# Kernel tuning notes

Hardware: AMD Instinct MI355X
Metric: run time of the kernel (lower is better)

Reference implementation:

```python
import jax, jax.numpy as jnp
import numpy as np

B, IN_CAPS, IN_DIM = 64, 2048, 16
NUM_CAPS, OUT_DIM = 32, 16
NUM_ROUTING = 3


def squash(v, axis=-1):
    # scale = |v|^2 / (1 + |v|^2) / |v|  (faithful to source, no epsilon)
    s2 = jnp.sum(jnp.square(v), axis=axis, keepdims=True)
    scale = s2 / (1.0 + s2) / jnp.sqrt(s2)
    return scale * v


def setup_inputs() -> dict:
    key = jax.random.key(0)
    k1, k2 = jax.random.split(key)
    inputs = jax.random.normal(k1, (B, IN_CAPS, IN_DIM), dtype=jnp.float32)
    # glorot-ish scaled transform matrices
    W = jax.random.normal(k2, (IN_CAPS, NUM_CAPS, IN_DIM, OUT_DIM), dtype=jnp.float32) * 0.05
    return {"inputs": inputs, "W": W}


def reference(inputs, W):
    # Prediction vectors u_hat[b,i,k,:] = inputs[b,i,:] @ W[i,k,:,:]
    u_hat = jnp.einsum('bid,ikdo->biko', inputs, W)  # [B, I, K, O]
    # Routing logits b (per-batch; source initializes from zeros and accumulates agreement)
    b = jnp.zeros(u_hat.shape[:3], dtype=u_hat.dtype)  # [B, I, K]
    v = None
    for i in range(NUM_ROUTING):
        c = jax.nn.softmax(b, axis=2)                      # coupling coeffs over output caps K
        s = jnp.einsum('bik,biko->bko', c, u_hat)          # weighted sum over input caps I
        v = squash(s)                                      # [B, K, O]
        if i != NUM_ROUTING - 1:
            b = b + jnp.einsum('biko,bko->bik', u_hat, v)  # agreement update
    return v  # [B, NUM_CAPS, OUT_DIM]
```

## Files before the change

kernel.cpp:

```cpp
#include <hip/hip_runtime.h>
#include <math.h>
#include <stdint.h>

#define NB 64
#define NI 2048
#define NK 32
#define ND 16

typedef _Float16 h2t   __attribute__((ext_vector_type(2)));
typedef _Float16 f16x4 __attribute__((ext_vector_type(4)));
typedef float    f32x4 __attribute__((ext_vector_type(4)));

#if defined(__has_builtin)
#if __has_builtin(__builtin_amdgcn_global_load_lds)
#define HAVE_GLL 1
#endif
#endif
#ifndef HAVE_GLL
#define HAVE_GLL 0
#endif

static __device__ __forceinline__ uint32_t pack_h2(float a, float b) {
    h2t p; p.x = (_Float16)a; p.y = (_Float16)b;
    return __builtin_bit_cast(uint32_t, p);
}

static __device__ __forceinline__ float swz_xor16(float x) {
    int v = __builtin_amdgcn_ds_swizzle(__builtin_bit_cast(int, x), 0x401F);
    return __builtin_bit_cast(float, v);
}
static __device__ __forceinline__ float xreduce_o(float p) {
    p += swz_xor16(p);
    p += __shfl_xor(p, 32);
    return p;
}

__global__ __launch_bounds__(256)
void conv_wx(const float* __restrict__ Wg, uint32_t* __restrict__ Wh,
             const float* __restrict__ X,  uint32_t* __restrict__ XT)
{
    __shared__ float tile[32 * 264];
    const int t = threadIdx.x;
    if (blockIdx.x < 2048) {
        const int i = blockIdx.x;
        const float4* src = (const float4*)(Wg + (size_t)i * 8192);
#pragma unroll
        for (int j = 0; j < 8; ++j) {
            const int f4 = t + j * 256;
            const int k  = f4 >> 6;
            const int r4 = f4 & 63;
            *(float4*)(&tile[k * 264 + r4 * 4]) = src[f4];
        }
        __syncthreads();
        const int T  = t >> 3;
        const int l0 = (t & 7) * 8;
        const float* s = tile + T * 264;
        uint2* dst = (uint2*)(Wh + (size_t)i * 4096) + T * 64 + l0;
#pragma unroll
        for (int n = 0; n < 8; ++n) {
            const int l = l0 + n;
            const int q = l >> 4, r = l & 15;
            uint2 u;
            u.x = pack_h2(s[(4 * q + 0) * 16 + r], s[(4 * q + 1) * 16 + r]);
            u.y = pack_h2(s[(4 * q + 2) * 16 + r], s[(4 * q + 3) * 16 + r]);
            dst[n] = u;
        }
    } else {
        const int g = (blockIdx.x - 2048) * 256 + t;
        const int b = g >> 11, i = g & 2047;
        const float4* src = (const float4*)(X + ((size_t)b * 2048 + i) * 16);
        const float4 f0 = src[0], f1 = src[1], f2 = src[2], f3 = src[3];
        uint4 o0, o1;
        o0.x = pack_h2(f0.x, f0.y); o0.y = pack_h2(f0.z, f0.w);
        o0.z = pack_h2(f1.x, f1.y); o0.w = pack_h2(f1.z, f1.w);
        o1.x = pack_h2(f2.x, f2.y); o1.y = pack_h2(f2.z, f2.w);
        o1.z = pack_h2(f3.x, f3.y); o1.w = pack_h2(f3.z, f3.w);
        uint4* dst = (uint4*)(XT + (size_t)i * 512 + b * 8);
        dst[0] = o0; dst[1] = o1;
    }
}

template<int VMODE>
__global__ __launch_bounds__(256, 2)
void caps_pass_m(const uint32_t* __restrict__ XT,
                 const uint32_t* __restrict__ Wh,
                 const float* __restrict__ V,
                 uint32_t* __restrict__ part_h)
{
    constexpr int IC = 16;
    constexpr int NP = IC / 2;
    __shared__ uint32_t Ws[2][2][4096];
    __shared__ uint32_t Xs[2048];
    __shared__ float    Ep[2][4][16];

    const int t = threadIdx.x;
    const int l = t & 63;
    const int w = t >> 6;
    const int r = l & 15;
    const int q = l >> 4;

    const int wg     = blockIdx.x;
    const int xcd    = wg & 7;
    const int slot   = wg >> 3;
    const int ichunk = xcd * 16 + (slot >> 2);
    const int bg     = slot & 3;
    const int i0 = ichunk * IC;
    const int b0 = bg * 16;

    f32x4 s_acc[8];
#pragma unroll
    for (int tt = 0; tt < 8; ++tt) s_acc[tt] = (f32x4){0.f, 0.f, 0.f, 0.f};

    f32x4 v_r[8];
    if constexpr (VMODE == 1) {
#pragma unroll
        for (int tt = 0; tt < 8; ++tt)
            v_r[tt] = *(const f32x4*)(V + ((size_t)(b0 + r) * NK + (8 * w + tt)) * 16 + 4 * q);
    }

    {
        const int ig = t >> 4, uu = t & 15;
        const uint4* src = (const uint4*)(XT + (size_t)(i0 + ig) * 512 + b0 * 8);
        *(uint4*)&Xs[ig * 128 + uu * 4]        = src[uu];
        *(uint4*)&Xs[ig * 128 + (uu + 16) * 4] = src[uu + 16];
    }

#if HAVE_GLL
#define STAGE_T(sl, half, tile)                                                \
    {                                                                          \
        const size_t ibase_ = (size_t)(tile) * 4096;                           \
        _Pragma("unroll")                                                      \
        for (int jj = 0; jj < 4; ++jj) {                                       \
            const int p = w * 4 + jj;                                          \
            __builtin_amdgcn_global_load_lds(                                  \
                (const __attribute__((address_space(1))) void*)(Wh + ibase_ + p * 256 + l * 4), \
                (__attribute__((address_space(3))) void*)&Ws[sl][half][p * 256], 16, 0, 0); \
        }                                                                      \
    }
#define BAR_W(n) asm volatile("s_waitcnt vmcnt(" #n ")\ns_barrier" ::: "memory");
#else
#define STAGE_T(sl, half, tile)                                                \
    {                                                                          \
        const size_t ibase_ = (size_t)(tile) * 4096;                           \
        _Pragma("unroll")                                                      \
        for (int jj = 0; jj < 4; ++jj) {                                       \
            const int p = w * 4 + jj;                                          \
            ((uint4*)&Ws[sl][half][p * 256])[l] = *(const uint4*)(Wh + ibase_ + p * 256 + l * 4); \
        }                                                                      \
    }
#define BAR_W(n) asm volatile("s_waitcnt vmcnt(0) lgkmcnt(0)\ns_barrier" ::: "memory");
#endif
#define BAR_E() asm volatile("s_waitcnt lgkmcnt(0)\ns_barrier" ::: "memory");

    __syncthreads();

    STAGE_T(0, 0, i0 + 0) STAGE_T(0, 1, i0 + 1)
    STAGE_T(1, 0, i0 + 2) STAGE_T(1, 1, i0 + 3)

    for (int j = 0; j < NP; ++j) {
        const int s = j & 1;
        if (j == 0) { BAR_W(8) } else { BAR_W(0) }

        if (j >= 1 && j + 1 < NP) {
            const int ns = s ^ 1;
            const int nt = i0 + 2 * (j + 1);
            STAGE_T(ns, 0, nt) STAGE_T(ns, 1, nt + 1)
        }

#pragma unroll
        for (int ia = 0; ia < 2; ++ia) {
            const int ii = 2 * j + ia;
            const f16x4 xb = *(const f16x4*)&Xs[ii * 128 + r * 8 + q * 2];

            if constexpr (VMODE == 0) {
#pragma unroll
                for (int tt = 0; tt < 8; ++tt) {
                    const f16x4 a = *(const f16x4*)&Ws[s][ia][(w * 8 + tt) * 128 + l * 2];
                    s_acc[tt] = __builtin_amdgcn_mfma_f32_16x16x16f16(a, xb, s_acc[tt], 0, 0, 0);
                }
            } else {
                f32x4 um[8];
#pragma unroll
                for (int tt = 0; tt < 8; ++tt) {
                    const f16x4 a = *(const f16x4*)&Ws[s][ia][(w * 8 + tt) * 128 + l * 2];
                    um[tt] = __builtin_amdgcn_mfma_f32_16x16x16f16(
                        a, xb, (f32x4){0.f, 0.f, 0.f, 0.f}, 0, 0, 0);
                }
                float e[8];
                float esp = 0.f;
#pragma unroll
                for (int tt = 0; tt < 8; ++tt) {
                    float p = um[tt][0] * v_r[tt][0];
                    p = fmaf(um[tt][1], v_r[tt][1], p);
                    p = fmaf(um[tt][2], v_r[tt][2], p);
                    p = fmaf(um[tt][3], v_r[tt][3], p);
                    p = xreduce_o(p);
                    e[tt] = __expf(p);
                    esp += e[tt];
                }
                if (q == 0) Ep[ia][w][r] = esp;
                BAR_E();
                const float es = Ep[ia][0][r] + Ep[ia][1][r]
                               + Ep[ia][2][r] + Ep[ia][3][r];
                const float ci = __builtin_amdgcn_rcpf(es);
#pragma unroll
                for (int tt = 0; tt < 8; ++tt) {
                    const float c = e[tt] * ci;
                    s_acc[tt][0] = fmaf(c, um[tt][0], s_acc[tt][0]);
                    s_acc[tt][1] = fmaf(c, um[tt][1], s_acc[tt][1]);
                    s_acc[tt][2] = fmaf(c, um[tt][2], s_acc[tt][2]);
                    s_acc[tt][3] = fmaf(c, um[tt][3], s_acc[tt][3]);
                }
            }
        }
    }
#undef STAGE_T
#undef BAR_W
#undef BAR_E

    uint32_t* base = part_h + (size_t)(bg * 128 + ichunk) * 4096 + r * 256 + 2 * q;
#pragma unroll
    for (int tt = 0; tt < 8; ++tt) {
        uint2 st;
        st.x = pack_h2(s_acc[tt][0], s_acc[tt][1]);
        st.y = pack_h2(s_acc[tt][2], s_acc[tt][3]);
        *(uint2*)(base + (8 * w + tt) * 8) = st;
    }
}

template<int RMODE>
__global__ __launch_bounds__(256)
void caps_reduce(const uint32_t* __restrict__ part_h,
                 const float* __restrict__ S0red,
                 float* __restrict__ S0out,
                 float* __restrict__ Vout)
{
    __shared__ float2 red[4][64];
    const int t   = threadIdx.x;
    const int jl  = t & 63;
    const int qc  = t >> 6;
    const int jb  = blockIdx.x * 64;
    const int j   = jb + jl;
    const int b   = j >> 8;
    const int bg  = b >> 4;
    const int loc = (b & 15) * 256 + (j & 255);
    const uint32_t* p = part_h + ((size_t)(bg * 128 + qc * 32)) * 4096 + loc;
    float sx = 0.f, sy = 0.f;
#pragma unroll 8
    for (int ic = 0; ic < 32; ++ic) {
        h2t v = __builtin_bit_cast(h2t, p[(size_t)ic * 4096]);
        sx += (float)v.x; sy += (float)v.y;
    }
    red[qc][jl] = make_float2(sx, sy);
    __syncthreads();
    if (t < 64) {
        const int jj = jb + t;
        float2 a0 = red[0][t], a1 = red[1][t], a2 = red[2][t], a3 = red[3][t];
        const float tx = a0.x + a1.x + a2.x + a3.x;
        const float ty = a0.y + a1.y + a2.y + a3.y;
        if constexpr (RMODE == 0) {
            S0out[2 * jj]     = tx;
            S0out[2 * jj + 1] = ty;
            const float vx = tx * (1.0f / 32.0f), vy = ty * (1.0f / 32.0f);
            float sq = vx * vx + vy * vy;
#pragma unroll
            for (int mask = 4; mask >= 1; mask >>= 1) sq += __shfl_xor(sq, mask);
            const float sc = sqrtf(sq) / (1.0f + sq);
            Vout[2 * jj]     = vx * sc;
            Vout[2 * jj + 1] = vy * sc;
        } else if constexpr (RMODE == 1) {
            const float v0x = S0red[2 * jj] * (1.0f / 32.0f);
            const float v0y = S0red[2 * jj + 1] * (1.0f / 32.0f);
            float sq0 = v0x * v0x + v0y * v0y;
#pragma unroll
            for (int mask = 4; mask >= 1; mask >>= 1) sq0 += __shfl_xor(sq0, mask);
            const float sc0 = sqrtf(sq0) / (1.0f + sq0);
            float sq1 = tx * tx + ty * ty;
#pragma unroll
            for (int mask = 4; mask >= 1; mask >>= 1) sq1 += __shfl_xor(sq1, mask);
            const float sc1 = sqrtf(sq1) / (1.0f + sq1);
            Vout[2 * jj]     = fmaf(v0x, sc0, tx * sc1);
            Vout[2 * jj + 1] = fmaf(v0y, sc0, ty * sc1);
        } else {
            float sq = tx * tx + ty * ty;
#pragma unroll
            for (int mask = 4; mask >= 1; mask >>= 1) sq += __shfl_xor(sq, mask);
            const float sc = sqrtf(sq) / (1.0f + sq);
            Vout[2 * jj]     = tx * sc;
            Vout[2 * jj + 1] = ty * sc;
        }
    }
}

template<int VMODE>
__global__ __launch_bounds__(256, 4)
void caps_pass_f32(const float* __restrict__ X,
                   const float* __restrict__ Wg,
                   const float* __restrict__ S0,
                   const float* __restrict__ S1,
                   float* __restrict__ Sout)
{
    constexpr int IC = 8;
    __shared__ float Ws[8192];
    __shared__ float Xs[2048];

    const int t   = threadIdx.x;
    const int kk  = t & 31;
    const int oh  = (t >> 5) & 1;
    const int bq4 = t >> 6;

    const int wg     = blockIdx.x;
    const int xcd    = wg & 7;
    const int slot   = wg >> 3;
    const int ichunk = xcd * 32 + (slot >> 2);
    const int bg     = slot & 3;
    const int i0 = ichunk * IC;
    const int b0 = bg * 16;

    float s_acc[4][8];
#pragma unroll
    for (int bb = 0; bb < 4; ++bb)
#pragma unroll
        for (int o = 0; o < 8; ++o) s_acc[bb][o] = 0.f;

    float v_r[4][8];
    if constexpr (VMODE >= 1) {
#pragma unroll
        for (int bb = 0; bb < 4; ++bb) {
            const int b = b0 + bq4 * 4 + bb;
            const float* p0 = S0 + ((size_t)b * NK + kk) * 16 + oh * 8;
            float4 a = *(const float4*)(p0);
            float4 c = *(const float4*)(p0 + 4);
            float val0[8] = {a.x,a.y,a.z,a.w,c.x,c.y,c.z,c.w};
            float sq0 = 0.f;
#pragma unroll
            for (int o = 0; o < 8; ++o) { val0[o] *= (1.0f/32.0f); sq0 = fmaf(val0[o], val0[o], sq0); }
            sq0 += __shfl_xor(sq0, 32);
            const float sc0 = sqrtf(sq0) / (1.0f + sq0);
#pragma unroll
            for (int o = 0; o < 8; ++o) v_r[bb][o] = val0[o] * sc0;
            if constexpr (VMODE == 2) {
                const float* p1 = S1 + ((size_t)b * NK + kk) * 16 + oh * 8;
                float4 a1 = *(const float4*)(p1);
                float4 c1 = *(const float4*)(p1 + 4);
                float val1[8] = {a1.x,a1.y,a1.z,a1.w,c1.x,c1.y,c1.z,c1.w};
                float sq1 = 0.f;
#pragma unroll
                for (int o = 0; o < 8; ++o) sq1 = fmaf(val1[o], val1[o], sq1);
                sq1 += __shfl_xor(sq1, 32);
                const float sc1 = sqrtf(sq1) / (1.0f + sq1);
#pragma unroll
                for (int o = 0; o < 8; ++o) v_r[bb][o] = fmaf(val1[o], sc1, v_r[bb][o]);
            }
        }
    }

    {
        const int xb   = t >> 4;
        const int xig  = t & 7;
        const int half = (t >> 3) & 1;
        const float* xp = X + (size_t)(b0 + xb) * (NI * ND) + (size_t)(i0 + xig) * ND + half * 8;
        float4 f0 = *(const float4*)(xp);
        float4 f1 = *(const float4*)(xp + 4);
        float vals[8] = {f0.x,f0.y,f0.z,f0.w,f1.x,f1.y,f1.z,f1.w};
        const int m = (xig & 7) << 3;
#pragma unroll
        for (int jj = 0; jj < 8; ++jj) {
            const int d = half * 8 + jj;
            Xs[xig * 256 + ((16 * d + xb) ^ m)] = vals[jj];
        }
    }

    for (int ii = 0; ii < IC; ++ii) {
        const int i = i0 + ii;
        __syncthreads();
        {
            const float4* wsrc = (const float4*)(Wg + (size_t)i * 8192);
#pragma unroll
            for (int j = 0; j < 8; ++j) {
                float4 val = wsrc[t + j * 256];
                const int k = (t >> 6) + 4 * j;
                ((float4*)Ws)[k * 64 + ((t & 63) ^ (k & 7))] = val;
            }
        }
        __syncthreads();

        const int xm = (ii & 7) << 3;
        float u[4][8];
        if constexpr (VMODE >= 1) {
#pragma unroll
            for (int bb = 0; bb < 4; ++bb)
#pragma unroll
                for (int o = 0; o < 8; ++o) u[bb][o] = 0.f;
        }
#pragma unroll
        for (int d = 0; d < 16; ++d) {
            const float4 x4 = *(const float4*)(&Xs[ii * 256 + ((16 * d + 4 * bq4) ^ xm)]);
            float wvv[8];
            {
                const float4 wA = ((const float4*)Ws)[kk * 64 + ((d * 4 + oh * 2)     ^ (kk & 7))];
                const float4 wB = ((const float4*)Ws)[kk * 64 + ((d * 4 + oh * 2 + 1) ^ (kk & 7))];
                wvv[0]=wA.x; wvv[1]=wA.y; wvv[2]=wA.z; wvv[3]=wA.w;
                wvv[4]=wB.x; wvv[5]=wB.y; wvv[6]=wB.z; wvv[7]=wB.w;
            }
            if constexpr (VMODE >= 1) {
#pragma unroll
                for (int o = 0; o < 8; ++o) {
                    u[0][o] = fmaf(x4.x, wvv[o], u[0][o]);
                    u[1][o] = fmaf(x4.y, wvv[o], u[1][o]);
                    u[2][o] = fmaf(x4.z, wvv[o], u[2][o]);
                    u[3][o] = fmaf(x4.w, wvv[o], u[3][o]);
                }
            } else {
#pragma unroll
                for (int o = 0; o < 8; ++o) {
                    s_acc[0][o] = fmaf(x4.x, wvv[o], s_acc[0][o]);
                    s_acc[1][o] = fmaf(x4.y, wvv[o], s_acc[1][o]);
                    s_acc[2][o] = fmaf(x4.z, wvv[o], s_acc[2][o]);
                    s_acc[3][o] = fmaf(x4.w, wvv[o], s_acc[3][o]);
                }
            }
        }

        if constexpr (VMODE >= 1) {
#pragma unroll
            for (int bb = 0; bb < 4; ++bb) {
                float lg = 0.f;
#pragma unroll
                for (int o = 0; o < 8; ++o) lg = fmaf(u[bb][o], v_r[bb][o], lg);
                lg += __shfl_xor(lg, 32);
                float m = lg;
#pragma unroll
                for (int mask = 16; mask >= 1; mask >>= 1)
                    m = fmaxf(m, __shfl_xor(m, mask));
                const float e = __expf(lg - m);
                float ssum = e;
#pragma unroll
                for (int mask = 16; mask >= 1; mask >>= 1)
                    ssum += __shfl_xor(ssum, mask);
                const float c = e / ssum;
#pragma unroll
                for (int o = 0; o < 8; ++o)
                    s_acc[bb][o] = fmaf(c, u[bb][o], s_acc[bb][o]);
            }
        }
    }

#pragma unroll
    for (int bb = 0; bb < 4; ++bb) {
        float* sp = Sout + ((size_t)(b0 + bq4 * 4 + bb) * NK + kk) * 16 + oh * 8;
#pragma unroll
        for (int o = 0; o < 8; ++o) atomicAdd(sp + o, s_acc[bb][o]);
    }
}

__global__ __launch_bounds__(256)
void squash_kernel(const float* __restrict__ S, float* __restrict__ Vout)
{
    const int idx = blockIdx.x * 256 + threadIdx.x;
    float val = S[idx];
    float sq = val * val;
#pragma unroll
    for (int mask = 8; mask >= 1; mask >>= 1) sq += __shfl_xor(sq, mask);
    const float sc = sqrtf(sq) / (1.0f + sq);
    Vout[idx] = val * sc;
}

extern "C" void kernel_launch(void* const* d_in, const int* in_sizes, int n_in,
                              void* d_out, int out_size, void* d_ws, size_t ws_size,
                              hipStream_t stream)
{
    const float* X  = (const float*)d_in[0];
    const float* Wg = (const float*)d_in[1];
    float* out = (float*)d_out;

    const size_t WHU   = (size_t)2048 * 4096;
    const size_t XHU   = (size_t)64 * 2048 * 8;
    const size_t PARTU = (size_t)512 * 4096;
    const size_t need  = (WHU + XHU + PARTU) * 4 + 3 * 32768 * 4;

    const dim3 blk(256), pgrid(512), rgrid(256);

    if (ws_size >= need) {
        uint32_t* Wh   = (uint32_t*)d_ws;
        uint32_t* XT   = Wh + WHU;
        uint32_t* part = XT + XHU;
        float* s0      = (float*)(part + PARTU);
        float* v0      = s0 + 32768;
        float* v01     = v0 + 32768;

        conv_wx<<<dim3(2560), blk, 0, stream>>>(Wg, Wh, X, XT);

        caps_pass_m<0><<<pgrid, blk, 0, stream>>>(XT, Wh, nullptr, part);
        caps_reduce<0><<<rgrid, blk, 0, stream>>>(part, nullptr, s0, v0);
        caps_pass_m<1><<<pgrid, blk, 0, stream>>>(XT, Wh, v0, part);
        caps_reduce<1><<<rgrid, blk, 0, stream>>>(part, s0, nullptr, v01);
        caps_pass_m<1><<<pgrid, blk, 0, stream>>>(XT, Wh, v01, part);
        caps_reduce<2><<<rgrid, blk, 0, stream>>>(part, nullptr, nullptr, out);
    } else {
        float* s0 = (float*)d_ws;
        float* s1 = s0 + 32768;
        float* s2 = s1 + 32768;
        hipMemsetAsync(d_ws, 0, (size_t)3 * 32768 * sizeof(float), stream);
        caps_pass_f32<0><<<dim3(1024), blk, 0, stream>>>(X, Wg, nullptr, nullptr, s0);
        caps_pass_f32<1><<<dim3(1024), blk, 0, stream>>>(X, Wg, s0, nullptr, s1);
        caps_pass_f32<2><<<dim3(1024), blk, 0, stream>>>(X, Wg, s0, s1, s2);
        squash_kernel<<<dim3(128), blk, 0, stream>>>(s2, out);
    }
}
```

Baseline: 93.57 us.

## Halve W staging buffer, pipeline per tile with wave-local waits, raise occupancy

Replaces the double-buffered pair-of-tiles W staging with a two-slot, one-tile-at-a-time ring. Each wave now waits only on its own global-to-LDS loads with vmcnt, because each wave reads only the W slice it loaded, so the workgroup barrier is gone. Halving the W buffer cuts LDS per block, and the launch bound rises from 2 to 3 blocks per CU to hide latency through more resident waves. The trade-off is a shallower prefetch distance (one tile ahead) and tighter register budget under the higher occupancy target.

```diff
diff --git a/kernel.cpp b/kernel.cpp
--- a/kernel.cpp
+++ b/kernel.cpp
@@ -81,15 +81,14 @@
 }
 
 template<int VMODE>
-__global__ __launch_bounds__(256, 2)
+__global__ __launch_bounds__(256, 3)
 void caps_pass_m(const uint32_t* __restrict__ XT,
                  const uint32_t* __restrict__ Wh,
                  const float* __restrict__ V,
                  uint32_t* __restrict__ part_h)
 {
     constexpr int IC = 16;
-    constexpr int NP = IC / 2;
-    __shared__ uint32_t Ws[2][2][4096];
+    __shared__ uint32_t Ws[2][4096];
     __shared__ uint32_t Xs[2048];
     __shared__ float    Ep[2][4][16];
 
@@ -126,7 +125,7 @@
     }
 
 #if HAVE_GLL
-#define STAGE_T(sl, half, tile)                                                \
+#define STAGE_T(sl, tile)                                                      \
     {                                                                          \
         const size_t ibase_ = (size_t)(tile) * 4096;                           \
         _Pragma("unroll")                                                      \
@@ -134,89 +133,89 @@
             const int p = w * 4 + jj;                                          \
             __builtin_amdgcn_global_load_lds(                                  \
                 (const __attribute__((address_space(1))) void*)(Wh + ibase_ + p * 256 + l * 4), \
-                (__attribute__((address_space(3))) void*)&Ws[sl][half][p * 256], 16, 0, 0); \
+                (__attribute__((address_space(3))) void*)&Ws[sl][p * 256], 16, 0, 0); \
         }                                                                      \
     }
-#define BAR_W(n) asm volatile("s_waitcnt vmcnt(" #n ")\ns_barrier" ::: "memory");
+#define WAIT_V(n) { asm volatile("s_waitcnt vmcnt(" #n ")" ::: "memory");      \
+                    __builtin_amdgcn_sched_barrier(0); }
 #else
-#define STAGE_T(sl, half, tile)                                                \
+#define STAGE_T(sl, tile)                                                      \
     {                                                                          \
         const size_t ibase_ = (size_t)(tile) * 4096;                           \
         _Pragma("unroll")                                                      \
         for (int jj = 0; jj < 4; ++jj) {                                       \
             const int p = w * 4 + jj;                                          \
-            ((uint4*)&Ws[sl][half][p * 256])[l] = *(const uint4*)(Wh + ibase_ + p * 256 + l * 4); \
+            ((uint4*)&Ws[sl][p * 256])[l] = *(const uint4*)(Wh + ibase_ + p * 256 + l * 4); \
         }                                                                      \
     }
-#define BAR_W(n) asm volatile("s_waitcnt vmcnt(0) lgkmcnt(0)\ns_barrier" ::: "memory");
+#define WAIT_V(n) { asm volatile("s_waitcnt vmcnt(0) lgkmcnt(0)" ::: "memory");\
+                    __builtin_amdgcn_sched_barrier(0); }
 #endif
 #define BAR_E() asm volatile("s_waitcnt lgkmcnt(0)\ns_barrier" ::: "memory");
+#define STAGE_GUARD() { asm volatile("s_waitcnt lgkmcnt(0)" ::: "memory");     \
+                        __builtin_amdgcn_sched_barrier(0); }
 
     __syncthreads();
 
-    STAGE_T(0, 0, i0 + 0) STAGE_T(0, 1, i0 + 1)
-    STAGE_T(1, 0, i0 + 2) STAGE_T(1, 1, i0 + 3)
-
-    for (int j = 0; j < NP; ++j) {
-        const int s = j & 1;
-        if (j == 0) { BAR_W(8) } else { BAR_W(0) }
-
-        if (j >= 1 && j + 1 < NP) {
-            const int ns = s ^ 1;
-            const int nt = i0 + 2 * (j + 1);
-            STAGE_T(ns, 0, nt) STAGE_T(ns, 1, nt + 1)
-        }
-
-#pragma unroll
-        for (int ia = 0; ia < 2; ++ia) {
-            const int ii = 2 * j + ia;
-            const f16x4 xb = *(const f16x4*)&Xs[ii * 128 + r * 8 + q * 2];
-
-            if constexpr (VMODE == 0) {
-#pragma unroll
-                for (int tt = 0; tt < 8; ++tt) {
-                    const f16x4 a = *(const f16x4*)&Ws[s][ia][(w * 8 + tt) * 128 + l * 2];
-                    s_acc[tt] = __builtin_amdgcn_mfma_f32_16x16x16f16(a, xb, s_acc[tt], 0, 0, 0);
-                }
-            } else {
-                f32x4 um[8];
-#pragma unroll
-                for (int tt = 0; tt < 8; ++tt) {
-                    const f16x4 a = *(const f16x4*)&Ws[s][ia][(w * 8 + tt) * 128 + l * 2];
-                    um[tt] = __builtin_amdgcn_mfma_f32_16x16x16f16(
-                        a, xb, (f32x4){0.f, 0.f, 0.f, 0.f}, 0, 0, 0);
-                }
-                float e[8];
-                float esp = 0.f;
-#pragma unroll
-                for (int tt = 0; tt < 8; ++tt) {
-                    float p = um[tt][0] * v_r[tt][0];
-                    p = fmaf(um[tt][1], v_r[tt][1], p);
-                    p = fmaf(um[tt][2], v_r[tt][2], p);
-                    p = fmaf(um[tt][3], v_r[tt][3], p);
-                    p = xreduce_o(p);
-                    e[tt] = __expf(p);
-                    esp += e[tt];
-                }
-                if (q == 0) Ep[ia][w][r] = esp;
-                BAR_E();
-                const float es = Ep[ia][0][r] + Ep[ia][1][r]
-                               + Ep[ia][2][r] + Ep[ia][3][r];
-                const float ci = __builtin_amdgcn_rcpf(es);
-#pragma unroll
-                for (int tt = 0; tt < 8; ++tt) {
-                    const float c = e[tt] * ci;
-                    s_acc[tt][0] = fmaf(c, um[tt][0], s_acc[tt][0]);
-                    s_acc[tt][1] = fmaf(c, um[tt][1], s_acc[tt][1]);
-                    s_acc[tt][2] = fmaf(c, um[tt][2], s_acc[tt][2]);
-                    s_acc[tt][3] = fmaf(c, um[tt][3], s_acc[tt][3]);
-                }
-            }
+    STAGE_T(0, i0)
+    STAGE_T(1, i0 + 1)
+
+    for (int ii = 0; ii < IC; ++ii) {
+        const int cur = ii & 1;
+        if (ii + 1 < IC) { WAIT_V(4) } else { WAIT_V(0) }
+
+        const f16x4 xb = *(const f16x4*)&Xs[ii * 128 + r * 8 + q * 2];
+
+        if constexpr (VMODE == 0) {
+#pragma unroll
+            for (int tt = 0; tt < 8; ++tt) {
+                const f16x4 a = *(const f16x4*)&Ws[cur][(w * 8 + tt) * 128 + l * 2];
+                s_acc[tt] = __builtin_amdgcn_mfma_f32_16x16x16f16(a, xb, s_acc[tt], 0, 0, 0);
+            }
+        } else {
+            f32x4 um[8];
+#pragma unroll
+            for (int tt = 0; tt < 8; ++tt) {
+                const f16x4 a = *(const f16x4*)&Ws[cur][(w * 8 + tt) * 128 + l * 2];
+                um[tt] = __builtin_amdgcn_mfma_f32_16x16x16f16(
+                    a, xb, (f32x4){0.f, 0.f, 0.f, 0.f}, 0, 0, 0);
+            }
+            float e[8];
+            float esp = 0.f;
+#pragma unroll
+            for (int tt = 0; tt < 8; ++tt) {
+                float p = um[tt][0] * v_r[tt][0];
+                p = fmaf(um[tt][1], v_r[tt][1], p);
+                p = fmaf(um[tt][2], v_r[tt][2], p);
+                p = fmaf(um[tt][3], v_r[tt][3], p);
+                p = xreduce_o(p);
+                e[tt] = __expf(p);
+                esp += e[tt];
+            }
+            if (q == 0) Ep[ii & 1][w][r] = esp;
+            BAR_E();
+            const float es = Ep[ii & 1][0][r] + Ep[ii & 1][1][r]
+                           + Ep[ii & 1][2][r] + Ep[ii & 1][3][r];
+            const float ci = __builtin_amdgcn_rcpf(es);
+#pragma unroll
+            for (int tt = 0; tt < 8; ++tt) {
+                const float c = e[tt] * ci;
+                s_acc[tt][0] = fmaf(c, um[tt][0], s_acc[tt][0]);
+                s_acc[tt][1] = fmaf(c, um[tt][1], s_acc[tt][1]);
+                s_acc[tt][2] = fmaf(c, um[tt][2], s_acc[tt][2]);
+                s_acc[tt][3] = fmaf(c, um[tt][3], s_acc[tt][3]);
+            }
+        }
+
+        if (ii + 2 < IC) {
+            STAGE_GUARD();
+            STAGE_T(cur, i0 + ii + 2)
         }
     }
 #undef STAGE_T
-#undef BAR_W
+#undef WAIT_V
 #undef BAR_E
+#undef STAGE_GUARD
 
     uint32_t* base = part_h + (size_t)(bg * 128 + ichunk) * 4096 + r * 256 + 2 * q;
 #pragma unroll
```

Result: slower. 95.68 us (+2.3%).
